# Optimization experiments

Hardware: AMD Instinct MI355X
Metric: run time of the kernel (lower is better)

## Reference

```python
import jax, jax.numpy as jnp
import numpy as np

B, T, H, D, O = 2, 2048, 16, 64, 1024  # batch, seq, heads, head_size, output_size
E = H * D


def setup_inputs() -> dict:
    key = jax.random.key(0)
    ks = jax.random.split(key, 8)
    return {
        "query": jax.random.normal(ks[0], (B, T, E), jnp.float32),
        "key": jax.random.normal(ks[1], (B, T, E), jnp.float32),
        "value": jax.random.normal(ks[2], (B, T, E), jnp.float32),
        "Wq": jax.random.normal(ks[3], (E, E), jnp.float32) * (E ** -0.5),
        "Wk": jax.random.normal(ks[4], (E, E), jnp.float32) * (E ** -0.5),
        "Wv": jax.random.normal(ks[5], (E, E), jnp.float32) * (E ** -0.5),
        "proj_kernel": jax.random.normal(ks[6], (H, D, O), jnp.float32) * (D ** -0.5),
        "proj_bias": jax.random.normal(ks[7], (O,), jnp.float32),
    }


def reference(query, key, value, Wq, Wk, Wv, proj_kernel, proj_bias):
    # Linear projections (torch nn.Linear: x @ W.T), then split heads
    q = (query @ Wq.T).reshape(B, T, H, D)
    k = (key @ Wk.T).reshape(B, T, H, D)
    v = (value @ Wv.T).reshape(B, T, H, D)
    q = q * (D ** -0.5)  # scale query by 1/sqrt(head_size)
    # logits: [B, H, N, M]
    logits = jnp.einsum("bnhd,bmhd->bhnm", q, k)
    attn_coef = jax.nn.softmax(logits, axis=-1)
    # attn @ V -> [B, N, H, D]
    mh = jnp.einsum("bhnm,bmhd->bnhd", attn_coef, v)
    # custom output projection with per-head kernel [H, D, O]
    out = jnp.einsum("bnhd,hdo->bno", mh, proj_kernel) + proj_bias
    return out, attn_coef
```

## Files before the change

### kernel.cpp

```cpp
#include <hip/hip_runtime.h>
#include <hip/hip_bf16.h>
#include <math.h>

#define B_ 2
#define T_ 2048
#define H_ 16
#define D_ 64
#define E_ 1024
#define O_ 1024
#define BT_ 4096

typedef __attribute__((ext_vector_type(8))) short bf8;
typedef __attribute__((ext_vector_type(4))) float f4;

static __device__ __forceinline__ unsigned short f2bf(float f) {
  unsigned u = __builtin_bit_cast(unsigned, f);
  u += 0x7FFFu + ((u >> 16) & 1u);
  return (unsigned short)(u >> 16);
}

static __device__ __forceinline__ uint4 cvt8(float4 a, float4 b) {
  union { unsigned short s[8]; uint4 v; } u;
  u.s[0] = f2bf(a.x); u.s[1] = f2bf(a.y); u.s[2] = f2bf(a.z); u.s[3] = f2bf(a.w);
  u.s[4] = f2bf(b.x); u.s[5] = f2bf(b.y); u.s[6] = f2bf(b.z); u.s[7] = f2bf(b.w);
  return u.v;
}

static __device__ __forceinline__ f4 mfma16(bf8 a, bf8 b, f4 c) {
  return __builtin_amdgcn_mfma_f32_16x16x32_bf16(a, b, c, 0, 0, 0);
}

__global__ __launch_bounds__(256) void qkv_gemm(const float* __restrict__ X,
                                                const float* __restrict__ W,
                                                unsigned short* __restrict__ dst,
                                                float scale) {
  __shared__ __align__(16) unsigned short lA[64 * 40];
  __shared__ __align__(16) unsigned short lB[128 * 40];
  const int tid = threadIdx.x;
  const int bx = blockIdx.x, by = blockIdx.y;
  const int lane = tid & 63, w = tid >> 6;
  const int l15 = lane & 15, qd = lane >> 4;
  const int wr = (w >> 1) * 32, wc = (w & 1) * 64;

  const int ar = tid >> 2, akc = (tid & 3) << 3;
  const int br = tid >> 1, bkc = (tid & 1) << 4;
  const float* aptr = X + (size_t)(bx * 64 + ar) * E_ + akc;
  const float* bptr = W + (size_t)(by * 128 + br) * E_ + bkc;

  f4 acc[2][4];
#pragma unroll
  for (int i = 0; i < 2; ++i)
#pragma unroll
    for (int j = 0; j < 4; ++j) acc[i][j] = (f4){0.f, 0.f, 0.f, 0.f};

  for (int k0 = 0; k0 < E_; k0 += 32) {
    __syncthreads();
    {
      const float4* p = (const float4*)aptr;
      *(uint4*)&lA[ar * 40 + akc] = cvt8(p[0], p[1]);
    }
    {
      const float4* p = (const float4*)bptr;
      *(uint4*)&lB[br * 40 + bkc] = cvt8(p[0], p[1]);
      *(uint4*)&lB[br * 40 + bkc + 8] = cvt8(p[2], p[3]);
    }
    aptr += 32; bptr += 32;
    __syncthreads();

    bf8 af[2], bfr[4];
#pragma unroll
    for (int rt = 0; rt < 2; ++rt)
      af[rt] = *(const bf8*)&lA[(wr + rt * 16 + l15) * 40 + qd * 8];
#pragma unroll
    for (int ct = 0; ct < 4; ++ct)
      bfr[ct] = *(const bf8*)&lB[(wc + ct * 16 + l15) * 40 + qd * 8];
#pragma unroll
    for (int rt = 0; rt < 2; ++rt)
#pragma unroll
      for (int ct = 0; ct < 4; ++ct)
        acc[rt][ct] = mfma16(af[rt], bfr[ct], acc[rt][ct]);
  }

#pragma unroll
  for (int rt = 0; rt < 2; ++rt)
#pragma unroll
    for (int ct = 0; ct < 4; ++ct)
#pragma unroll
      for (int r = 0; r < 4; ++r) {
        int m = bx * 64 + wr + rt * 16 + qd * 4 + r;
        int n = by * 128 + wc + ct * 16 + l15;
        int b = m >> 11, t = m & 2047;
        int h = n >> 6, d = n & 63;
        dst[((size_t)(b * H_ + h) * T_ + t) * D_ + d] = f2bf(acc[rt][ct][r] * scale);
      }
}

__global__ __launch_bounds__(256) void transpose_v(const unsigned short* __restrict__ vh,
                                                   unsigned short* __restrict__ vt) {
  __shared__ __align__(16) unsigned short lT[64 * 72];
  const int tid = threadIdx.x;
  const int bh = blockIdx.x >> 5;
  const int t0 = (blockIdx.x & 31) * 64;
  const unsigned short* src = vh + (size_t)bh * T_ * D_ + (size_t)t0 * D_;
#pragma unroll
  for (int i = 0; i < 2; ++i) {
    int c = tid + i * 256;
    int row = c >> 3, dc = (c & 7) << 3;
    *(uint4*)&lT[row * 72 + dc] = *(const uint4*)(src + row * D_ + dc);
  }
  __syncthreads();
  unsigned short* dstp = vt + (size_t)bh * D_ * T_;
#pragma unroll
  for (int i = 0; i < 2; ++i) {
    int c = tid + i * 256;
    int d = c >> 3, tc = (c & 7) << 3;
    union { unsigned short s[8]; uint4 v; } u;
#pragma unroll
    for (int j = 0; j < 8; ++j) u.s[j] = lT[(tc + j) * 72 + d];
    *(uint4*)(dstp + (size_t)d * T_ + t0 + tc) = u.v;
  }
}

__global__ __launch_bounds__(256) void transpose_proj(const float* __restrict__ pk,
                                                      unsigned short* __restrict__ pt) {
  __shared__ __align__(16) unsigned short lT[64 * 72];
  const int tid = threadIdx.x;
  const int hd0 = (blockIdx.x >> 4) * 64;
  const int o0 = (blockIdx.x & 15) * 64;
#pragma unroll
  for (int i = 0; i < 2; ++i) {
    int c = tid + i * 256;
    int row = c >> 3, oc = (c & 7) << 3;
    const float4* p = (const float4*)(pk + (size_t)(hd0 + row) * O_ + o0 + oc);
    *(uint4*)&lT[row * 72 + oc] = cvt8(p[0], p[1]);
  }
  __syncthreads();
#pragma unroll
  for (int i = 0; i < 2; ++i) {
    int c = tid + i * 256;
    int orow = c >> 3, hc = (c & 7) << 3;
    union { unsigned short s[8]; uint4 v; } u;
#pragma unroll
    for (int j = 0; j < 8; ++j) u.s[j] = lT[(hc + j) * 72 + orow];
    *(uint4*)(pt + (size_t)(o0 + orow) * E_ + hd0 + hc) = u.v;
  }
}

__global__ __launch_bounds__(256) void attention(const unsigned short* __restrict__ qh,
                                                 const unsigned short* __restrict__ kh,
                                                 const unsigned short* __restrict__ vt,
                                                 float* __restrict__ attn,
                                                 unsigned short* __restrict__ mh) {
  __shared__ __align__(16) unsigned short lQ[64 * 72];
  __shared__ __align__(16) unsigned short lK[32 * 72];
  __shared__ __align__(16) unsigned short lV[64 * 40];
  __shared__ __align__(16) unsigned short lP[4 * 16 * 40];

  const int tid = threadIdx.x;
  const int bh = blockIdx.x >> 5;
  const int n0 = (blockIdx.x & 31) * 64;
  const int lane = tid & 63, w = tid >> 6;
  const int l15 = lane & 15, qd = lane >> 4;

  const unsigned short* qbase = qh + (size_t)bh * T_ * D_ + (size_t)n0 * D_;
  const unsigned short* kbase = kh + (size_t)bh * T_ * D_;
  const unsigned short* vbase = vt + (size_t)bh * D_ * T_;

#pragma unroll
  for (int i = 0; i < 2; ++i) {
    int c = tid + i * 256;
    int row = c >> 3, dc = (c & 7) << 3;
    *(uint4*)&lQ[row * 72 + dc] = *(const uint4*)(qbase + row * D_ + dc);
  }
  __syncthreads();

  const bf8 aq0 = *(const bf8*)&lQ[(w * 16 + l15) * 72 + qd * 8];
  const bf8 aq1 = *(const bf8*)&lQ[(w * 16 + l15) * 72 + 32 + qd * 8];

  const int kr = tid >> 3, kc = (tid & 7) << 3;
  const int vr = tid >> 2, vc = (tid & 3) << 3;

  float mloc[4] = {-INFINITY, -INFINITY, -INFINITY, -INFINITY};
  float lsum[4] = {0.f, 0.f, 0.f, 0.f};

  for (int m0 = 0; m0 < T_; m0 += 32) {
    __syncthreads();
    *(uint4*)&lK[kr * 72 + kc] = *(const uint4*)(kbase + (size_t)(m0 + kr) * D_ + kc);
    __syncthreads();
    f4 s0 = (f4){0.f, 0.f, 0.f, 0.f}, s1 = (f4){0.f, 0.f, 0.f, 0.f};
    bf8 b00 = *(const bf8*)&lK[l15 * 72 + qd * 8];
    bf8 b01 = *(const bf8*)&lK[l15 * 72 + 32 + qd * 8];
    bf8 b10 = *(const bf8*)&lK[(16 + l15) * 72 + qd * 8];
    bf8 b11 = *(const bf8*)&lK[(16 + l15) * 72 + 32 + qd * 8];
    s0 = mfma16(aq0, b00, s0); s0 = mfma16(aq1, b01, s0);
    s1 = mfma16(aq0, b10, s1); s1 = mfma16(aq1, b11, s1);
#pragma unroll
    for (int r = 0; r < 4; ++r) {
      float v0 = s0[r], v1 = s1[r];
      float nm = fmaxf(mloc[r], fmaxf(v0, v1));
      lsum[r] = lsum[r] * __expf(mloc[r] - nm) + __expf(v0 - nm) + __expf(v1 - nm);
      mloc[r] = nm;
    }
  }

  float mrow[4], invl[4];
#pragma unroll
  for (int r = 0; r < 4; ++r) {
    float mx = mloc[r];
#pragma unroll
    for (int off = 1; off < 16; off <<= 1) mx = fmaxf(mx, __shfl_xor(mx, off));
    float ls = lsum[r] * __expf(mloc[r] - mx);
#pragma unroll
    for (int off = 1; off < 16; off <<= 1) ls += __shfl_xor(ls, off);
    mrow[r] = mx;
    invl[r] = 1.0f / ls;
  }

  f4 o[4];
#pragma unroll
  for (int dt = 0; dt < 4; ++dt) o[dt] = (f4){0.f, 0.f, 0.f, 0.f};

  float* attnrow = attn + ((size_t)bh * T_ + n0) * T_;
  unsigned short* lPw = lP + w * 640;

  for (int m0 = 0; m0 < T_; m0 += 32) {
    __syncthreads();
    *(uint4*)&lK[kr * 72 + kc] = *(const uint4*)(kbase + (size_t)(m0 + kr) * D_ + kc);
    *(uint4*)&lV[vr * 40 + vc] = *(const uint4*)(vbase + (size_t)vr * T_ + m0 + vc);
    __syncthreads();
    f4 s0 = (f4){0.f, 0.f, 0.f, 0.f}, s1 = (f4){0.f, 0.f, 0.f, 0.f};
    bf8 b00 = *(const bf8*)&lK[l15 * 72 + qd * 8];
    bf8 b01 = *(const bf8*)&lK[l15 * 72 + 32 + qd * 8];
    bf8 b10 = *(const bf8*)&lK[(16 + l15) * 72 + qd * 8];
    bf8 b11 = *(const bf8*)&lK[(16 + l15) * 72 + 32 + qd * 8];
    s0 = mfma16(aq0, b00, s0); s0 = mfma16(aq1, b01, s0);
    s1 = mfma16(aq0, b10, s1); s1 = mfma16(aq1, b11, s1);
#pragma unroll
    for (int r = 0; r < 4; ++r) {
      int row = w * 16 + qd * 4 + r;
      float p0 = __expf(s0[r] - mrow[r]) * invl[r];
      float p1 = __expf(s1[r] - mrow[r]) * invl[r];
      attnrow[(size_t)row * T_ + m0 + l15] = p0;
      attnrow[(size_t)row * T_ + m0 + 16 + l15] = p1;
      lPw[(qd * 4 + r) * 40 + l15] = f2bf(p0);
      lPw[(qd * 4 + r) * 40 + 16 + l15] = f2bf(p1);
    }
    bf8 ap = *(const bf8*)&lPw[l15 * 40 + qd * 8];
#pragma unroll
    for (int dt = 0; dt < 4; ++dt) {
      bf8 bv = *(const bf8*)&lV[(dt * 16 + l15) * 40 + qd * 8];
      o[dt] = mfma16(ap, bv, o[dt]);
    }
  }

  const int b = bh >> 4, h = bh & 15;
#pragma unroll
  for (int dt = 0; dt < 4; ++dt)
#pragma unroll
    for (int r = 0; r < 4; ++r) {
      int t = n0 + w * 16 + qd * 4 + r;
      int d = dt * 16 + l15;
      mh[(size_t)(b * T_ + t) * E_ + h * D_ + d] = f2bf(o[dt][r]);
    }
}

__global__ __launch_bounds__(256) void out_gemm(const unsigned short* __restrict__ A,
                                                const unsigned short* __restrict__ Bm,
                                                const float* __restrict__ bias,
                                                float* __restrict__ Cout) {
  __shared__ __align__(16) unsigned short lA[64 * 40];
  __shared__ __align__(16) unsigned short lB[128 * 40];
  const int tid = threadIdx.x;
  const int bx = blockIdx.x, by = blockIdx.y;
  const int lane = tid & 63, w = tid >> 6;
  const int l15 = lane & 15, qd = lane >> 4;
  const int wr = (w >> 1) * 32, wc = (w & 1) * 64;

  const int ar = tid >> 2, akc = (tid & 3) << 3;
  const unsigned short* aptr = A + (size_t)(bx * 64 + ar) * E_ + akc;

  f4 acc[2][4];
#pragma unroll
  for (int i = 0; i < 2; ++i)
#pragma unroll
    for (int j = 0; j < 4; ++j) acc[i][j] = (f4){0.f, 0.f, 0.f, 0.f};

  for (int k0 = 0; k0 < E_; k0 += 32) {
    __syncthreads();
    *(uint4*)&lA[ar * 40 + akc] = *(const uint4*)aptr;
#pragma unroll
    for (int i = 0; i < 2; ++i) {
      int c = tid + i * 256;
      int br = c >> 2, bkc = (c & 3) << 3;
      *(uint4*)&lB[br * 40 + bkc] =
          *(const uint4*)(Bm + (size_t)(by * 128 + br) * E_ + k0 + bkc);
    }
    aptr += 32;
    __syncthreads();

    bf8 af[2], bfr[4];
#pragma unroll
    for (int rt = 0; rt < 2; ++rt)
      af[rt] = *(const bf8*)&lA[(wr + rt * 16 + l15) * 40 + qd * 8];
#pragma unroll
    for (int ct = 0; ct < 4; ++ct)
      bfr[ct] = *(const bf8*)&lB[(wc + ct * 16 + l15) * 40 + qd * 8];
#pragma unroll
    for (int rt = 0; rt < 2; ++rt)
#pragma unroll
      for (int ct = 0; ct < 4; ++ct)
        acc[rt][ct] = mfma16(af[rt], bfr[ct], acc[rt][ct]);
  }

#pragma unroll
  for (int ct = 0; ct < 4; ++ct) {
    int n = by * 128 + wc + ct * 16 + l15;
    float bv = bias[n];
#pragma unroll
    for (int rt = 0; rt < 2; ++rt)
#pragma unroll
      for (int r = 0; r < 4; ++r) {
        int m = bx * 64 + wr + rt * 16 + qd * 4 + r;
        Cout[(size_t)m * O_ + n] = acc[rt][ct][r] + bv;
      }
  }
}

extern "C" void kernel_launch(void* const* d_in, const int* in_sizes, int n_in,
                              void* d_out, int out_size, void* d_ws, size_t ws_size,
                              hipStream_t stream) {
  const float* query = (const float*)d_in[0];
  const float* key_i = (const float*)d_in[1];
  const float* value = (const float*)d_in[2];
  const float* Wq = (const float*)d_in[3];
  const float* Wk = (const float*)d_in[4];
  const float* Wv = (const float*)d_in[5];
  const float* pk = (const float*)d_in[6];
  const float* pb = (const float*)d_in[7];

  float* out = (float*)d_out;
  float* attn = out + (size_t)BT_ * O_;

  unsigned short* ws = (unsigned short*)d_ws;
  unsigned short* qh = ws;
  unsigned short* kh = qh + (size_t)4194304;
  unsigned short* vh = kh + (size_t)4194304;
  unsigned short* vtb = vh + (size_t)4194304;
  unsigned short* pt = vtb + (size_t)4194304;
  unsigned short* mhb = vh;

  dim3 g(64, 8), blk(256, 1, 1);
  hipLaunchKernelGGL(qkv_gemm, g, blk, 0, stream, query, Wq, qh, 0.125f);
  hipLaunchKernelGGL(qkv_gemm, g, blk, 0, stream, key_i, Wk, kh, 1.0f);
  hipLaunchKernelGGL(qkv_gemm, g, blk, 0, stream, value, Wv, vh, 1.0f);
  hipLaunchKernelGGL(transpose_v, dim3(1024), blk, 0, stream, vh, vtb);
  hipLaunchKernelGGL(transpose_proj, dim3(256), blk, 0, stream, pk, pt);
  hipLaunchKernelGGL(attention, dim3(1024), blk, 0, stream, qh, kh, vtb, attn, mhb);
  hipLaunchKernelGGL(out_gemm, g, blk, 0, stream, mhb, pt, pb, out);
}
```

Measured before the change: 837.6 us.

## Merge QKV GEMMs, widen attention tiles, use exp2 and vectorized nontemporal stores

The three QKV projection launches become one launch over a z-dimension, and the query scale folds in log2(e) so softmax can use the hardware exp2 instruction. The attention kernel now processes 64-key tiles, computes transposed scores (K as the A operand), and keeps a per-lane online max/sum merged by shuffles across quads. Attention probabilities are written as float4 nontemporal stores with packed bf16 conversion into LDS, and the output GEMM also uses nontemporal stores. The aim is to cut launch overhead, exp cost, scattered stores and syncs per key, at the cost of more LDS per block and reliance on inline asm.

New measurement: 794.9 us. 1.05x faster.

```diff
diff --git a/kernel.cpp b/kernel.cpp
--- a/kernel.cpp
+++ b/kernel.cpp
@@ -9,6 +9,7 @@
 #define E_ 1024
 #define O_ 1024
 #define BT_ 4096
+#define SCALE_Q 0.18033688011f
 
 typedef __attribute__((ext_vector_type(8))) short bf8;
 typedef __attribute__((ext_vector_type(4))) float f4;
@@ -30,12 +31,35 @@
   return __builtin_amdgcn_mfma_f32_16x16x32_bf16(a, b, c, 0, 0, 0);
 }
 
-__global__ __launch_bounds__(256) void qkv_gemm(const float* __restrict__ X,
-                                                const float* __restrict__ W,
-                                                unsigned short* __restrict__ dst,
-                                                float scale) {
+static __device__ __forceinline__ float ex2(float x) {
+  float r;
+  asm("v_exp_f32 %0, %1" : "=v"(r) : "v"(x));
+  return r;
+}
+
+static __device__ __forceinline__ unsigned cvtpk_bf(float lo, float hi) {
+  unsigned r;
+  asm("v_cvt_pk_bf16_f32 %0, %1, %2" : "=v"(r) : "v"(lo), "v"(hi));
+  return r;
+}
+
+__global__ __launch_bounds__(256) void qkv_gemm(const float* __restrict__ Xq,
+                                                const float* __restrict__ Xk,
+                                                const float* __restrict__ Xv,
+                                                const float* __restrict__ Wq,
+                                                const float* __restrict__ Wk,
+                                                const float* __restrict__ Wv,
+                                                unsigned short* __restrict__ dq,
+                                                unsigned short* __restrict__ dk,
+                                                unsigned short* __restrict__ dv) {
   __shared__ __align__(16) unsigned short lA[64 * 40];
   __shared__ __align__(16) unsigned short lB[128 * 40];
+  const int z = blockIdx.z;
+  const float* X = (z == 0) ? Xq : (z == 1) ? Xk : Xv;
+  const float* W = (z == 0) ? Wq : (z == 1) ? Wk : Wv;
+  unsigned short* dst = (z == 0) ? dq : (z == 1) ? dk : dv;
+  const float scale = (z == 0) ? SCALE_Q : 1.0f;
+
   const int tid = threadIdx.x;
   const int bx = blockIdx.x, by = blockIdx.y;
   const int lane = tid & 63, w = tid >> 6;
@@ -151,10 +175,9 @@
                                                  const unsigned short* __restrict__ vt,
                                                  float* __restrict__ attn,
                                                  unsigned short* __restrict__ mh) {
-  __shared__ __align__(16) unsigned short lQ[64 * 72];
-  __shared__ __align__(16) unsigned short lK[32 * 72];
-  __shared__ __align__(16) unsigned short lV[64 * 40];
-  __shared__ __align__(16) unsigned short lP[4 * 16 * 40];
+  __shared__ __align__(16) unsigned short lK[64 * 72];
+  __shared__ __align__(16) unsigned short lV[64 * 72];
+  __shared__ __align__(16) unsigned short lP[4 * 16 * 72];
 
   const int tid = threadIdx.x;
   const int bh = blockIdx.x >> 5;
@@ -162,94 +185,106 @@
   const int lane = tid & 63, w = tid >> 6;
   const int l15 = lane & 15, qd = lane >> 4;
 
-  const unsigned short* qbase = qh + (size_t)bh * T_ * D_ + (size_t)n0 * D_;
+  const unsigned short* qbase = qh + ((size_t)bh * T_ + n0) * D_;
   const unsigned short* kbase = kh + (size_t)bh * T_ * D_;
   const unsigned short* vbase = vt + (size_t)bh * D_ * T_;
 
-#pragma unroll
-  for (int i = 0; i < 2; ++i) {
-    int c = tid + i * 256;
-    int row = c >> 3, dc = (c & 7) << 3;
-    *(uint4*)&lQ[row * 72 + dc] = *(const uint4*)(qbase + row * D_ + dc);
-  }
-  __syncthreads();
-
-  const bf8 aq0 = *(const bf8*)&lQ[(w * 16 + l15) * 72 + qd * 8];
-  const bf8 aq1 = *(const bf8*)&lQ[(w * 16 + l15) * 72 + 32 + qd * 8];
-
-  const int kr = tid >> 3, kc = (tid & 7) << 3;
-  const int vr = tid >> 2, vc = (tid & 3) << 3;
-
-  float mloc[4] = {-INFINITY, -INFINITY, -INFINITY, -INFINITY};
-  float lsum[4] = {0.f, 0.f, 0.f, 0.f};
-
-  for (int m0 = 0; m0 < T_; m0 += 32) {
-    __syncthreads();
-    *(uint4*)&lK[kr * 72 + kc] = *(const uint4*)(kbase + (size_t)(m0 + kr) * D_ + kc);
-    __syncthreads();
-    f4 s0 = (f4){0.f, 0.f, 0.f, 0.f}, s1 = (f4){0.f, 0.f, 0.f, 0.f};
-    bf8 b00 = *(const bf8*)&lK[l15 * 72 + qd * 8];
-    bf8 b01 = *(const bf8*)&lK[l15 * 72 + 32 + qd * 8];
-    bf8 b10 = *(const bf8*)&lK[(16 + l15) * 72 + qd * 8];
-    bf8 b11 = *(const bf8*)&lK[(16 + l15) * 72 + 32 + qd * 8];
-    s0 = mfma16(aq0, b00, s0); s0 = mfma16(aq1, b01, s0);
-    s1 = mfma16(aq0, b10, s1); s1 = mfma16(aq1, b11, s1);
-#pragma unroll
-    for (int r = 0; r < 4; ++r) {
-      float v0 = s0[r], v1 = s1[r];
-      float nm = fmaxf(mloc[r], fmaxf(v0, v1));
-      lsum[r] = lsum[r] * __expf(mloc[r] - nm) + __expf(v0 - nm) + __expf(v1 - nm);
-      mloc[r] = nm;
-    }
-  }
-
-  float mrow[4], invl[4];
-#pragma unroll
-  for (int r = 0; r < 4; ++r) {
-    float mx = mloc[r];
-#pragma unroll
-    for (int off = 1; off < 16; off <<= 1) mx = fmaxf(mx, __shfl_xor(mx, off));
-    float ls = lsum[r] * __expf(mloc[r] - mx);
-#pragma unroll
-    for (int off = 1; off < 16; off <<= 1) ls += __shfl_xor(ls, off);
-    mrow[r] = mx;
-    invl[r] = 1.0f / ls;
-  }
+  const bf8 aq0 = *(const bf8*)(qbase + (w * 16 + l15) * D_ + qd * 8);
+  const bf8 aq1 = *(const bf8*)(qbase + (w * 16 + l15) * D_ + 32 + qd * 8);
+
+  const int srow = tid >> 3, scol = (tid & 7) << 3;
+
+  float mL = -INFINITY, lL = 0.f;
+  for (int m0 = 0; m0 < T_; m0 += 64) {
+    __syncthreads();
+#pragma unroll
+    for (int i = 0; i < 2; ++i) {
+      int row = srow + i * 32;
+      *(uint4*)&lK[row * 72 + scol] = *(const uint4*)(kbase + (size_t)(m0 + row) * D_ + scol);
+    }
+    __syncthreads();
+    f4 s[4];
+#pragma unroll
+    for (int kk = 0; kk < 4; ++kk) {
+      bf8 k0 = *(const bf8*)&lK[(kk * 16 + l15) * 72 + qd * 8];
+      bf8 k1 = *(const bf8*)&lK[(kk * 16 + l15) * 72 + 32 + qd * 8];
+      f4 t = (f4){0.f, 0.f, 0.f, 0.f};
+      t = mfma16(k0, aq0, t);
+      t = mfma16(k1, aq1, t);
+      s[kk] = t;
+    }
+    float tm = s[0][0];
+#pragma unroll
+    for (int kk = 0; kk < 4; ++kk)
+#pragma unroll
+      for (int r = 0; r < 4; ++r) tm = fmaxf(tm, s[kk][r]);
+    float nm = fmaxf(mL, tm);
+    lL *= ex2(mL - nm);
+    mL = nm;
+#pragma unroll
+    for (int kk = 0; kk < 4; ++kk)
+#pragma unroll
+      for (int r = 0; r < 4; ++r) lL += ex2(s[kk][r] - mL);
+  }
+
+  float mrow = mL, lrow = lL;
+#pragma unroll
+  for (int off = 16; off < 64; off <<= 1) {
+    float om = __shfl_xor(mrow, off);
+    float ol = __shfl_xor(lrow, off);
+    float nm = fmaxf(mrow, om);
+    lrow = lrow * ex2(mrow - nm) + ol * ex2(om - nm);
+    mrow = nm;
+  }
+  const float invl = 1.0f / lrow;
 
   f4 o[4];
 #pragma unroll
   for (int dt = 0; dt < 4; ++dt) o[dt] = (f4){0.f, 0.f, 0.f, 0.f};
 
-  float* attnrow = attn + ((size_t)bh * T_ + n0) * T_;
-  unsigned short* lPw = lP + w * 640;
-
-  for (int m0 = 0; m0 < T_; m0 += 32) {
-    __syncthreads();
-    *(uint4*)&lK[kr * 72 + kc] = *(const uint4*)(kbase + (size_t)(m0 + kr) * D_ + kc);
-    *(uint4*)&lV[vr * 40 + vc] = *(const uint4*)(vbase + (size_t)vr * T_ + m0 + vc);
-    __syncthreads();
-    f4 s0 = (f4){0.f, 0.f, 0.f, 0.f}, s1 = (f4){0.f, 0.f, 0.f, 0.f};
-    bf8 b00 = *(const bf8*)&lK[l15 * 72 + qd * 8];
-    bf8 b01 = *(const bf8*)&lK[l15 * 72 + 32 + qd * 8];
-    bf8 b10 = *(const bf8*)&lK[(16 + l15) * 72 + qd * 8];
-    bf8 b11 = *(const bf8*)&lK[(16 + l15) * 72 + 32 + qd * 8];
-    s0 = mfma16(aq0, b00, s0); s0 = mfma16(aq1, b01, s0);
-    s1 = mfma16(aq0, b10, s1); s1 = mfma16(aq1, b11, s1);
-#pragma unroll
-    for (int r = 0; r < 4; ++r) {
-      int row = w * 16 + qd * 4 + r;
-      float p0 = __expf(s0[r] - mrow[r]) * invl[r];
-      float p1 = __expf(s1[r] - mrow[r]) * invl[r];
-      attnrow[(size_t)row * T_ + m0 + l15] = p0;
-      attnrow[(size_t)row * T_ + m0 + 16 + l15] = p1;
-      lPw[(qd * 4 + r) * 40 + l15] = f2bf(p0);
-      lPw[(qd * 4 + r) * 40 + 16 + l15] = f2bf(p1);
-    }
-    bf8 ap = *(const bf8*)&lPw[l15 * 40 + qd * 8];
+  float* attnrow = attn + ((size_t)bh * T_ + n0 + w * 16 + l15) * T_ + qd * 4;
+  unsigned short* lPw = lP + w * 16 * 72;
+
+  for (int m0 = 0; m0 < T_; m0 += 64) {
+    __syncthreads();
+#pragma unroll
+    for (int i = 0; i < 2; ++i) {
+      int row = srow + i * 32;
+      *(uint4*)&lK[row * 72 + scol] = *(const uint4*)(kbase + (size_t)(m0 + row) * D_ + scol);
+      *(uint4*)&lV[row * 72 + scol] = *(const uint4*)(vbase + (size_t)row * T_ + m0 + scol);
+    }
+    __syncthreads();
+    f4 s[4];
+#pragma unroll
+    for (int kk = 0; kk < 4; ++kk) {
+      bf8 k0 = *(const bf8*)&lK[(kk * 16 + l15) * 72 + qd * 8];
+      bf8 k1 = *(const bf8*)&lK[(kk * 16 + l15) * 72 + 32 + qd * 8];
+      f4 t = (f4){0.f, 0.f, 0.f, 0.f};
+      t = mfma16(k0, aq0, t);
+      t = mfma16(k1, aq1, t);
+      s[kk] = t;
+    }
+#pragma unroll
+    for (int kk = 0; kk < 4; ++kk) {
+      float p0 = ex2(s[kk][0] - mrow) * invl;
+      float p1 = ex2(s[kk][1] - mrow) * invl;
+      float p2 = ex2(s[kk][2] - mrow) * invl;
+      float p3 = ex2(s[kk][3] - mrow) * invl;
+      f4 pf = (f4){p0, p1, p2, p3};
+      __builtin_nontemporal_store(pf, (f4*)(attnrow + m0 + kk * 16));
+      uint2 pb;
+      pb.x = cvtpk_bf(p0, p1);
+      pb.y = cvtpk_bf(p2, p3);
+      *(uint2*)&lPw[l15 * 72 + kk * 16 + qd * 4] = pb;
+    }
+    bf8 ap0 = *(const bf8*)&lPw[l15 * 72 + qd * 8];
+    bf8 ap1 = *(const bf8*)&lPw[l15 * 72 + 32 + qd * 8];
 #pragma unroll
     for (int dt = 0; dt < 4; ++dt) {
-      bf8 bv = *(const bf8*)&lV[(dt * 16 + l15) * 40 + qd * 8];
-      o[dt] = mfma16(ap, bv, o[dt]);
+      bf8 bv0 = *(const bf8*)&lV[(dt * 16 + l15) * 72 + qd * 8];
+      bf8 bv1 = *(const bf8*)&lV[(dt * 16 + l15) * 72 + 32 + qd * 8];
+      o[dt] = mfma16(ap0, bv0, o[dt]);
+      o[dt] = mfma16(ap1, bv1, o[dt]);
     }
   }
 
@@ -321,7 +356,7 @@
 #pragma unroll
       for (int r = 0; r < 4; ++r) {
         int m = bx * 64 + wr + rt * 16 + qd * 4 + r;
-        Cout[(size_t)m * O_ + n] = acc[rt][ct][r] + bv;
+        __builtin_nontemporal_store(acc[rt][ct][r] + bv, &Cout[(size_t)m * O_ + n]);
       }
   }
 }
@@ -349,12 +384,11 @@
   unsigned short* pt = vtb + (size_t)4194304;
   unsigned short* mhb = vh;
 
-  dim3 g(64, 8), blk(256, 1, 1);
-  hipLaunchKernelGGL(qkv_gemm, g, blk, 0, stream, query, Wq, qh, 0.125f);
-  hipLaunchKernelGGL(qkv_gemm, g, blk, 0, stream, key_i, Wk, kh, 1.0f);
-  hipLaunchKernelGGL(qkv_gemm, g, blk, 0, stream, value, Wv, vh, 1.0f);
+  dim3 blk(256, 1, 1);
+  hipLaunchKernelGGL(qkv_gemm, dim3(64, 8, 3), blk, 0, stream,
+                     query, key_i, value, Wq, Wk, Wv, qh, kh, vh);
   hipLaunchKernelGGL(transpose_v, dim3(1024), blk, 0, stream, vh, vtb);
   hipLaunchKernelGGL(transpose_proj, dim3(256), blk, 0, stream, pk, pt);
   hipLaunchKernelGGL(attention, dim3(1024), blk, 0, stream, qh, kh, vtb, attn, mhb);
-  hipLaunchKernelGGL(out_gemm, g, blk, 0, stream, mhb, pt, pb, out);
-}
+  hipLaunchKernelGGL(out_gemm, dim3(64, 8), blk, 0, stream, mhb, pt, pb, out);
+}
```
